# Optimization experiments

Measured on AMD Instinct MI355X. Metric: run time of the kernel, lower is better.

The kernel has to match this reference:

```python
import jax, jax.numpy as jnp
import numpy as np

S = 128            # image_size
NF = 64            # nf (channels)
B, N = 16, 1
DIM = S * S // 16  # 1024
HEADS = max(1, S // 16)  # 8
DH = DIM // HEADS  # 128


def setup_inputs() -> dict:
    key = jax.random.key(0)
    ks = jax.random.split(key, 10)
    sc = lambda fan_in: 1.0 / np.sqrt(fan_in)
    return {
        "x": jax.random.normal(ks[0], (B, N, NF, S, S), dtype=jnp.float32),
        "We": jax.random.uniform(ks[1], (DIM, S * S), jnp.float32, -sc(S * S), sc(S * S)),
        "be": jax.random.uniform(ks[2], (DIM,), jnp.float32, -sc(S * S), sc(S * S)),
        "pos": jax.random.normal(ks[3], (1, NF, DIM), dtype=jnp.float32),
        "Wq": jax.random.uniform(ks[4], (DIM, DIM), jnp.float32, -sc(DIM), sc(DIM)),
        "Wk": jax.random.uniform(ks[5], (NF, NF), jnp.float32, -sc(NF), sc(NF)),
        "Wv": jax.random.uniform(ks[6], (DIM, DIM), jnp.float32, -sc(DIM), sc(DIM)),
        "Wo": jax.random.uniform(ks[7], (S * S, DIM), jnp.float32, -sc(DIM), sc(DIM)),
        "bo": jax.random.uniform(ks[8], (S * S,), jnp.float32, -sc(DIM), sc(DIM)),
    }


def reference(x, We, be, pos, Wq, Wk, Wv, Wo, bo):
    b, n, C, H, W = x.shape
    bn = b * n
    xf = x.reshape(bn, C, H * W)                       # [BN, C, S^2]
    xe = jnp.einsum('bcp,dp->bcd', xf, We) + be + pos  # [BN, C, DIM]
    # q projection -> heads -> avgpool over head dim (AvgPool1d(dh) == mean)
    q = jnp.einsum('bcd,ed->bce', xe, Wq).reshape(bn, C, HEADS, DH)
    q = q.transpose(0, 2, 1, 3)                        # [BN, H, C, dh]
    q = q.mean(axis=-1)                                # [BN, H, C]
    k = jax.nn.sigmoid(jnp.einsum('bhc,fc->bhf', q, Wk))  # [BN, H, C]
    v = jnp.einsum('bcd,ed->bce', xe, Wv).reshape(bn, C, HEADS, DH)
    v = v.transpose(0, 2, 1, 3)                        # [BN, H, C, dh]
    # diag_embed(k) @ v == per-channel elementwise scale
    out = k[..., None] * v                             # [BN, H, C, dh]
    out = out.transpose(0, 2, 1, 3).reshape(bn, C, DIM)
    out = jnp.einsum('bcd,pd->bcp', out, Wo) + bo      # [BN, C, S^2]
    return out.reshape(b, n, C, H, W)
```

## Files before the change

kernel.cpp:

```cpp
#include <hip/hip_runtime.h>
#include <cstdint>
#include <cmath>


typedef __attribute__((ext_vector_type(8))) short short8;
typedef __attribute__((ext_vector_type(4))) float f32x4;

#define DIMD 1024
#define NCH  64
#define NHEAD 8
#define DHEAD 128

typedef __attribute__((address_space(1))) unsigned int gu32;
typedef __attribute__((address_space(3))) unsigned int lu32;

__device__ __forceinline__ void gload_lds16(const void* g, void* l) {
  __builtin_amdgcn_global_load_lds((gu32*)g, (lu32*)l, 16, 0, 0);
}

__device__ __forceinline__ unsigned short f2bf(float f) {
  union { float f; unsigned u; } a; a.f = f;
  unsigned u = a.u;
  unsigned r = (u + 0x7fffu + ((u >> 16) & 1u)) >> 16;
  return (unsigned short)r;
}
__device__ __forceinline__ float bf2f(unsigned short h) {
  union { unsigned u; float f; } a; a.u = ((unsigned)h) << 16; return a.f;
}

__global__ __launch_bounds__(256) void cvt_bf16_kernel(
    const float* __restrict__ in, unsigned short* __restrict__ out, int n8) {
  int i = blockIdx.x * 256 + threadIdx.x;
  if (i >= n8) return;
  const float4* p = (const float4*)in + (size_t)i * 2;
  float4 f0 = p[0], f1 = p[1];
  uint4 u;
  u.x = (unsigned)f2bf(f0.x) | ((unsigned)f2bf(f0.y) << 16);
  u.y = (unsigned)f2bf(f0.z) | ((unsigned)f2bf(f0.w) << 16);
  u.z = (unsigned)f2bf(f1.x) | ((unsigned)f2bf(f1.y) << 16);
  u.w = (unsigned)f2bf(f1.z) | ((unsigned)f2bf(f1.w) << 16);
  ((uint4*)out)[i] = u;
}

__global__ __launch_bounds__(256) void wqm2_kernel(
    const float* __restrict__ Wq, float* __restrict__ wqm) {
  int h = blockIdx.x >> 3, dbase = (blockIdx.x & 7) * 128;
  int d = threadIdx.x & 127, eh = threadIdx.x >> 7;
  const float* p = Wq + ((size_t)(h * DHEAD + eh * 64)) * DIMD + dbase + d;
  float s = 0.f;
  #pragma unroll 8
  for (int e = 0; e < 64; ++e) s += p[(size_t)e * DIMD];
  __shared__ float red[2][128];
  red[eh][d] = s;
  __syncthreads();
  if (eh == 0)
    wqm[h * DIMD + dbase + d] = (red[0][d] + red[1][d]) * (1.0f / DHEAD);
}

__global__ __launch_bounds__(256) void qk2_kernel(
    const unsigned short* __restrict__ xe, const float* __restrict__ wqm,
    const float* __restrict__ Wk, float* __restrict__ kout) {
  int b = blockIdx.x, h = blockIdx.y;
  int c = threadIdx.x & 63, dq = threadIdx.x >> 6;
  __shared__ float red[64][4];
  __shared__ float qs[64];
  const uint4* xr = (const uint4*)(xe + ((size_t)(b * NCH + c)) * DIMD + dq * 256);
  const float* wr = wqm + h * DIMD + dq * 256;
  float s = 0.f;
  #pragma unroll 4
  for (int i = 0; i < 32; ++i) {
    uint4 v = xr[i];
    s += bf2f((unsigned short)(v.x & 0xffff)) * wr[i * 8 + 0];
    s += bf2f((unsigned short)(v.x >> 16))    * wr[i * 8 + 1];
    s += bf2f((unsigned short)(v.y & 0xffff)) * wr[i * 8 + 2];
    s += bf2f((unsigned short)(v.y >> 16))    * wr[i * 8 + 3];
    s += bf2f((unsigned short)(v.z & 0xffff)) * wr[i * 8 + 4];
    s += bf2f((unsigned short)(v.z >> 16))    * wr[i * 8 + 5];
    s += bf2f((unsigned short)(v.w & 0xffff)) * wr[i * 8 + 6];
    s += bf2f((unsigned short)(v.w >> 16))    * wr[i * 8 + 7];
  }
  red[c][dq] = s;
  __syncthreads();
  if (dq == 0) qs[c] = red[c][0] + red[c][1] + red[c][2] + red[c][3];
  __syncthreads();
  int f = c;
  float s2 = 0.f;
  #pragma unroll
  for (int i = 0; i < 16; ++i) {
    int cc = dq * 16 + i;
    s2 += qs[cc] * Wk[f * NCH + cc];
  }
  red[f][dq] = s2;
  __syncthreads();
  if (dq == 0) {
    float q = red[f][0] + red[f][1] + red[f][2] + red[f][3];
    kout[(b * NHEAD + h) * NCH + f] = 1.f / (1.f + expf(-q));
  }
}

template<int MODE, int LAYOUT>
__global__ __launch_bounds__(256) void gemm_db(
    const unsigned short* __restrict__ A, const unsigned short* __restrict__ B,
    float* __restrict__ C, const float* __restrict__ bias,
    int M, int N, int K, int Ksub)
{
  __shared__ __align__(16) unsigned short As[2][128][32];
  __shared__ __align__(16) unsigned short Bs[2][128][32];

  const int bid = blockIdx.x;
  int m0, n0, kz;
  if (LAYOUT == 0) {
    kz = bid & 7; int r = bid >> 3; n0 = (r & 7) * 128; m0 = (r >> 3) * 128;
  } else if (LAYOUT == 1) {
    kz = (bid & 7) | (((bid >> 3) & 1) << 3);
    int r = bid >> 4; n0 = (r & 7) * 128; m0 = (r >> 3) * 128;
  } else {
    int nlo = bid & 7, nhi = bid >> 6;
    m0 = ((bid >> 3) & 7) * 128; n0 = (nlo + 8 * nhi) * 128; kz = 0;
  }

  const int tid  = threadIdx.x;
  const int lane = tid & 63, wave = tid >> 6;
  const int kbeg = kz * Ksub;
  const int lrow = lane >> 2;
  const int lcol = (lane & 3) * 8;
  const int q = lane >> 4, rl = lane & 15;
  const int wr = (wave >> 1) * 64, wc = (wave & 1) * 64;

  const unsigned short* ga = A + (size_t)(m0 + wave * 32 + lrow) * K + kbeg + lcol;
  const unsigned short* gb = B + (size_t)(n0 + wave * 32 + lrow) * K + kbeg + lcol;

  f32x4 acc[4][4] = {};

  gload_lds16(ga,                  &As[0][wave * 32][0]);
  gload_lds16(ga + (size_t)16 * K, &As[0][wave * 32 + 16][0]);
  gload_lds16(gb,                  &Bs[0][wave * 32][0]);
  gload_lds16(gb + (size_t)16 * K, &Bs[0][wave * 32 + 16][0]);
  ga += 32; gb += 32;

  int p = 0;
  for (int k0 = 0; k0 < Ksub; k0 += 32) {
    __syncthreads();
    if (k0 + 32 < Ksub) {
      gload_lds16(ga,                  &As[p ^ 1][wave * 32][0]);
      gload_lds16(ga + (size_t)16 * K, &As[p ^ 1][wave * 32 + 16][0]);
      gload_lds16(gb,                  &Bs[p ^ 1][wave * 32][0]);
      gload_lds16(gb + (size_t)16 * K, &Bs[p ^ 1][wave * 32 + 16][0]);
      ga += 32; gb += 32;
    }

    short8 af[4], bf[4];
    #pragma unroll
    for (int i = 0; i < 4; ++i)
      af[i] = *(const short8*)&As[p][wr + i * 16 + rl][q * 8];
    #pragma unroll
    for (int j = 0; j < 4; ++j)
      bf[j] = *(const short8*)&Bs[p][wc + j * 16 + rl][q * 8];
    #pragma unroll
    for (int i = 0; i < 4; ++i)
      #pragma unroll
      for (int j = 0; j < 4; ++j)
        acc[i][j] = __builtin_amdgcn_mfma_f32_16x16x32_bf16(af[i], bf[j], acc[i][j], 0, 0, 0);

    p ^= 1;
  }

  const size_t zoff = (MODE == 3) ? (size_t)kz * (size_t)M * (size_t)N : 0;
  #pragma unroll
  for (int i = 0; i < 4; ++i) {
    #pragma unroll
    for (int j = 0; j < 4; ++j) {
      #pragma unroll
      for (int r = 0; r < 4; ++r) {
        int row = m0 + wr + i * 16 + q * 4 + r;
        int col = n0 + wc + j * 16 + rl;
        if (MODE == 3) {
          C[zoff + (size_t)row * N + col] = acc[i][j][r];
        } else {
          C[(size_t)row * N + col] = acc[i][j][r] + bias[col];
        }
      }
    }
  }
}

template<int NS>
__global__ __launch_bounds__(256) void reduce1_kernel(
    const float* __restrict__ part, const float* __restrict__ be,
    const float* __restrict__ pos, unsigned short* __restrict__ xe) {
  int i = blockIdx.x * 256 + threadIdx.x;
  size_t base = (size_t)i * 4;
  int row = i >> 8, col = (i & 255) * 4;
  float4 s = {0.f, 0.f, 0.f, 0.f};
  #pragma unroll
  for (int sk = 0; sk < NS; ++sk) {
    float4 p = *(const float4*)(part + (size_t)sk * (DIMD * DIMD) + base);
    s.x += p.x; s.y += p.y; s.z += p.z; s.w += p.w;
  }
  float4 bv = *(const float4*)(be + col);
  float4 pv = *(const float4*)(pos + (size_t)(row & 63) * DIMD + col);
  uint2 u;
  u.x = (unsigned)f2bf(s.x + bv.x + pv.x) | ((unsigned)f2bf(s.y + bv.y + pv.y) << 16);
  u.y = (unsigned)f2bf(s.z + bv.z + pv.z) | ((unsigned)f2bf(s.w + bv.w + pv.w) << 16);
  *(uint2*)(xe + base) = u;
}

template<int NS>
__global__ __launch_bounds__(256) void reduce2_kernel(
    const float* __restrict__ part, const float* __restrict__ kv,
    unsigned short* __restrict__ t) {
  int i = blockIdx.x * 256 + threadIdx.x;
  size_t base = (size_t)i * 4;
  int row = i >> 8, col = (i & 255) * 4;
  float4 s = {0.f, 0.f, 0.f, 0.f};
  #pragma unroll
  for (int sk = 0; sk < NS; ++sk) {
    float4 p = *(const float4*)(part + (size_t)sk * (DIMD * DIMD) + base);
    s.x += p.x; s.y += p.y; s.z += p.z; s.w += p.w;
  }
  float sc = kv[((row >> 6) * NHEAD + (col >> 7)) * NCH + (row & 63)];
  uint2 u;
  u.x = (unsigned)f2bf(s.x * sc) | ((unsigned)f2bf(s.y * sc) << 16);
  u.y = (unsigned)f2bf(s.z * sc) | ((unsigned)f2bf(s.w * sc) << 16);
  *(uint2*)(t + base) = u;
}

template<int MODE, bool ABF16, int BM, int BN>
__global__ __launch_bounds__(256) void gemm_bt(
    const void* __restrict__ Ap, const float* __restrict__ B,
    void* __restrict__ C, const float* __restrict__ bias,
    const float* __restrict__ posp, const float* __restrict__ ksc,
    int M, int N, int K)
{
  constexpr int BK = 32;
  constexpr int LDR = BK + 8;
  __shared__ __align__(16) unsigned short As[BM][LDR];
  __shared__ __align__(16) unsigned short Bs[BN][LDR];

  const int tid = threadIdx.x;
  const int m0 = blockIdx.y * BM;
  const int n0 = blockIdx.x * BN;
  constexpr int EA = BM * BK / 256;
  constexpr int EB = BN * BK / 256;
  constexpr int MI = BM / 32;
  constexpr int NI = BN / 32;
  const int lane = tid & 63, wave = tid >> 6;
  const int wr = (wave >> 1) * (BM / 2);
  const int wc = (wave & 1) * (BN / 2);
  const int q = lane >> 4, rl = lane & 15;

  f32x4 acc[MI][NI] = {};

  for (int k0 = 0; k0 < K; k0 += BK) {
    {
      constexpr int CPR = BK / EA;
      int row = tid / CPR;
      int cs  = (tid % CPR) * EA;
      if (ABF16) {
        const unsigned short* a = (const unsigned short*)Ap + (size_t)(m0 + row) * K + k0 + cs;
        #pragma unroll
        for (int v = 0; v < EA / 8; ++v)
          *(uint4*)&As[row][cs + v * 8] = *(const uint4*)(a + v * 8);
      } else {
        const float* a = (const float*)Ap + (size_t)(m0 + row) * K + k0 + cs;
        #pragma unroll
        for (int v = 0; v < EA / 8; ++v) {
          float4 f0 = *(const float4*)(a + v * 8);
          float4 f1 = *(const float4*)(a + v * 8 + 4);
          uint4 u;
          u.x = (unsigned)f2bf(f0.x) | ((unsigned)f2bf(f0.y) << 16);
          u.y = (unsigned)f2bf(f0.z) | ((unsigned)f2bf(f0.w) << 16);
          u.z = (unsigned)f2bf(f1.x) | ((unsigned)f2bf(f1.y) << 16);
          u.w = (unsigned)f2bf(f1.z) | ((unsigned)f2bf(f1.w) << 16);
          *(uint4*)&As[row][cs + v * 8] = u;
        }
      }
    }
    {
      constexpr int CPR = BK / EB;
      int row = tid / CPR;
      int cs  = (tid % CPR) * EB;
      const float* b = B + (size_t)(n0 + row) * K + k0 + cs;
      #pragma unroll
      for (int v = 0; v < EB / 8; ++v) {
        float4 f0 = *(const float4*)(b + v * 8);
        float4 f1 = *(const float4*)(b + v * 8 + 4);
        uint4 u;
        u.x = (unsigned)f2bf(f0.x) | ((unsigned)f2bf(f0.y) << 16);
        u.y = (unsigned)f2bf(f0.z) | ((unsigned)f2bf(f0.w) << 16);
        u.z = (unsigned)f2bf(f1.x) | ((unsigned)f2bf(f1.y) << 16);
        u.w = (unsigned)f2bf(f1.z) | ((unsigned)f2bf(f1.w) << 16);
        *(uint4*)&Bs[row][cs + v * 8] = u;
      }
    }
    __syncthreads();

    short8 af[MI], bf[NI];
    #pragma unroll
    for (int i = 0; i < MI; ++i)
      af[i] = *(const short8*)&As[wr + i * 16 + rl][q * 8];
    #pragma unroll
    for (int j = 0; j < NI; ++j)
      bf[j] = *(const short8*)&Bs[wc + j * 16 + rl][q * 8];
    #pragma unroll
    for (int i = 0; i < MI; ++i)
      #pragma unroll
      for (int j = 0; j < NI; ++j)
        acc[i][j] = __builtin_amdgcn_mfma_f32_16x16x32_bf16(af[i], bf[j], acc[i][j], 0, 0, 0);

    __syncthreads();
  }

  #pragma unroll
  for (int i = 0; i < MI; ++i) {
    #pragma unroll
    for (int j = 0; j < NI; ++j) {
      #pragma unroll
      for (int r = 0; r < 4; ++r) {
        int row = m0 + wr + i * 16 + q * 4 + r;
        int col = n0 + wc + j * 16 + rl;
        float v = acc[i][j][r];
        if (MODE == 0) {
          v += bias[col] + posp[(size_t)(row & 63) * DIMD + col];
          ((unsigned short*)C)[(size_t)row * N + col] = f2bf(v);
        } else if (MODE == 1) {
          v *= ksc[((row >> 6) * NHEAD + (col >> 7)) * NCH + (row & 63)];
          ((unsigned short*)C)[(size_t)row * N + col] = f2bf(v);
        } else {
          ((float*)C)[(size_t)row * N + col] = v + bias[col];
        }
      }
    }
  }
}

__global__ void wqm_kernel(const float* __restrict__ Wq, float* __restrict__ wqm) {
  int h = blockIdx.x;
  for (int d = threadIdx.x; d < DIMD; d += 256) {
    float s = 0.f;
    const float* p = Wq + (size_t)h * DHEAD * DIMD + d;
    #pragma unroll 4
    for (int e = 0; e < DHEAD; ++e) s += p[(size_t)e * DIMD];
    wqm[h * DIMD + d] = s * (1.0f / DHEAD);
  }
}
__global__ void qk_kernel(const unsigned short* __restrict__ xe,
                          const float* __restrict__ wqm,
                          const float* __restrict__ Wk,
                          float* __restrict__ kout) {
  int b = blockIdx.x;
  __shared__ float qs[NHEAD][NCH];
  for (int t = threadIdx.x; t < NHEAD * NCH; t += 256) {
    int h = t >> 6, c = t & 63;
    const unsigned short* xr = xe + (size_t)(b * NCH + c) * DIMD;
    const float* wr = wqm + h * DIMD;
    float s = 0.f;
    #pragma unroll 8
    for (int d = 0; d < DIMD; ++d) s += bf2f(xr[d]) * wr[d];
    qs[h][c] = s;
  }
  __syncthreads();
  for (int t = threadIdx.x; t < NHEAD * NCH; t += 256) {
    int h = t >> 6, f = t & 63;
    float s = 0.f;
    #pragma unroll
    for (int c = 0; c < NCH; ++c) s += qs[h][c] * Wk[f * NCH + c];
    kout[b * (NHEAD * NCH) + h * NCH + f] = 1.f / (1.f + expf(-s));
  }
}

extern "C" void kernel_launch(void* const* d_in, const int* in_sizes, int n_in,
                              void* d_out, int out_size, void* d_ws, size_t ws_size,
                              hipStream_t stream) {
  const float* x   = (const float*)d_in[0];
  const float* We  = (const float*)d_in[1];
  const float* be  = (const float*)d_in[2];
  const float* pos = (const float*)d_in[3];
  const float* Wq  = (const float*)d_in[4];
  const float* Wk  = (const float*)d_in[5];
  const float* Wv  = (const float*)d_in[6];
  const float* Wo  = (const float*)d_in[7];
  const float* bo  = (const float*)d_in[8];
  float* out = (float*)d_out;

  const size_t MB = 1u << 20;
  const size_t WS16 = 102 * MB + 64 * 1024;
  const size_t WS8  = 70 * MB + 64 * 1024;

  if (ws_size >= WS16) {
    char* ws = (char*)d_ws;
    unsigned short* We_bf = (unsigned short*)(ws + 0);
    unsigned short* Wo_bf = (unsigned short*)(ws + 32 * MB);
    unsigned short* x_bf  = (unsigned short*)(ws + 64 * MB);
    unsigned short* Wv_bf = (unsigned short*)(ws + 96 * MB);
    unsigned short* xe    = (unsigned short*)(ws + 98 * MB);
    unsigned short* t     = (unsigned short*)(ws + 100 * MB);
    float* wqm = (float*)(ws + 102 * MB);
    float* kv  = (float*)(ws + 102 * MB + 32 * 1024);

    float* part1 = (float*)d_out;
    float* part2 = (float*)d_out;

    cvt_bf16_kernel<<<dim3(8192), 256, 0, stream>>>(x,  x_bf,  16777216 / 8);
    cvt_bf16_kernel<<<dim3(8192), 256, 0, stream>>>(We, We_bf, 16777216 / 8);
    cvt_bf16_kernel<<<dim3(512),  256, 0, stream>>>(Wv, Wv_bf, 1048576 / 8);
    cvt_bf16_kernel<<<dim3(8192), 256, 0, stream>>>(Wo, Wo_bf, 16777216 / 8);
    wqm2_kernel<<<dim3(64), 256, 0, stream>>>(Wq, wqm);

    gemm_db<3, 1><<<dim3(1024), 256, 0, stream>>>(
        x_bf, We_bf, part1, nullptr, 1024, 1024, 16384, 1024);
    reduce1_kernel<16><<<dim3(1024), 256, 0, stream>>>(part1, be, pos, xe);

    qk2_kernel<<<dim3(16, 8), 256, 0, stream>>>(xe, wqm, Wk, kv);

    gemm_db<3, 0><<<dim3(512), 256, 0, stream>>>(
        xe, Wv_bf, part2, nullptr, 1024, 1024, 1024, 128);
    reduce2_kernel<8><<<dim3(1024), 256, 0, stream>>>(part2, kv, t);

    gemm_db<2, 2><<<dim3(1024), 256, 0, stream>>>(
        t, Wo_bf, out, bo, 1024, 16384, 1024, 1024);
  } else if (ws_size >= WS8) {
    char* ws = (char*)d_ws;
    unsigned short* We_bf = (unsigned short*)(ws + 0);
    unsigned short* Wo_bf = (unsigned short*)(ws + 32 * MB);
    unsigned short* Wv_bf = (unsigned short*)(ws + 64 * MB);
    unsigned short* xe    = (unsigned short*)(ws + 66 * MB);
    unsigned short* t     = (unsigned short*)(ws + 68 * MB);
    float* wqm = (float*)(ws + 70 * MB);
    float* kv  = (float*)(ws + 70 * MB + 32 * 1024);

    char* ob = (char*)d_out;
    unsigned short* x_bf  = (unsigned short*)(ob + 0);
    float* part1 = (float*)(ob + 32 * MB);
    float* part2 = (float*)(ob + 0);

    cvt_bf16_kernel<<<dim3(8192), 256, 0, stream>>>(x,  x_bf,  16777216 / 8);
    cvt_bf16_kernel<<<dim3(8192), 256, 0, stream>>>(We, We_bf, 16777216 / 8);
    cvt_bf16_kernel<<<dim3(512),  256, 0, stream>>>(Wv, Wv_bf, 1048576 / 8);
    cvt_bf16_kernel<<<dim3(8192), 256, 0, stream>>>(Wo, Wo_bf, 16777216 / 8);
    wqm2_kernel<<<dim3(64), 256, 0, stream>>>(Wq, wqm);

    gemm_db<3, 0><<<dim3(512), 256, 0, stream>>>(
        x_bf, We_bf, part1, nullptr, 1024, 1024, 16384, 2048);
    reduce1_kernel<8><<<dim3(1024), 256, 0, stream>>>(part1, be, pos, xe);

    qk2_kernel<<<dim3(16, 8), 256, 0, stream>>>(xe, wqm, Wk, kv);

    gemm_db<3, 0><<<dim3(512), 256, 0, stream>>>(
        xe, Wv_bf, part2, nullptr, 1024, 1024, 1024, 128);
    reduce2_kernel<8><<<dim3(1024), 256, 0, stream>>>(part2, kv, t);

    gemm_db<2, 2><<<dim3(1024), 256, 0, stream>>>(
        t, Wo_bf, out, bo, 1024, 16384, 1024, 1024);
  } else {
    char* ws = (char*)d_ws;
    unsigned short* xe = (unsigned short*)ws;
    unsigned short* t  = (unsigned short*)(ws + (2u << 20));
    float* wqm = (float*)(ws + (4u << 20));
    float* kv  = (float*)(ws + (4u << 20) + (32u << 10));

    wqm_kernel<<<dim3(NHEAD), 256, 0, stream>>>(Wq, wqm);
    gemm_bt<0, false, 64, 64><<<dim3(16, 16), 256, 0, stream>>>(
        x, We, xe, be, pos, nullptr, 1024, 1024, 16384);
    qk_kernel<<<dim3(16), 256, 0, stream>>>(xe, wqm, Wk, kv);
    gemm_bt<1, true, 64, 64><<<dim3(16, 16), 256, 0, stream>>>(
        xe, Wv, t, nullptr, nullptr, kv, 1024, 1024, 1024);
    gemm_bt<2, true, 128, 128><<<dim3(128, 8), 256, 0, stream>>>(
        t, Wo, out, bo, nullptr, nullptr, 1024, 16384, 1024);
  }
}
```

Measured before the change: 368.6 us.

## Add 256x256 8-wave pipelined bf16 GEMM and fuse prep conversion kernels

Introduces a new GEMM kernel with 512 threads, 256x256 output tiles, K-step 64, swizzled LDS staging via global_load_lds, and a four-phase schedule that interleaves loads of the next tile with MFMA work on the current one. It is used for the two large GEMMs (x·We split-K and t·Wo) instead of the old 128x128 kernel. The five fp32-to-bf16 conversion and Wq-mean launches are merged into one kernel to cut launch overhead. The larger tiles reduce global traffic per FLOP but raise register and LDS pressure and leave fewer blocks to fill the CUs.

```diff
diff --git a/kernel.cpp b/kernel.cpp
--- a/kernel.cpp
+++ b/kernel.cpp
@@ -28,10 +28,8 @@
   union { unsigned u; float f; } a; a.u = ((unsigned)h) << 16; return a.f;
 }
 
-__global__ __launch_bounds__(256) void cvt_bf16_kernel(
-    const float* __restrict__ in, unsigned short* __restrict__ out, int n8) {
-  int i = blockIdx.x * 256 + threadIdx.x;
-  if (i >= n8) return;
+__device__ __forceinline__ void cvt8_body(const float* __restrict__ in,
+                                          unsigned short* __restrict__ out, int i) {
   const float4* p = (const float4*)in + (size_t)i * 2;
   float4 f0 = p[0], f1 = p[1];
   uint4 u;
@@ -40,6 +38,44 @@
   u.z = (unsigned)f2bf(f1.x) | ((unsigned)f2bf(f1.y) << 16);
   u.w = (unsigned)f2bf(f1.z) | ((unsigned)f2bf(f1.w) << 16);
   ((uint4*)out)[i] = u;
+}
+
+__global__ __launch_bounds__(256) void cvt_bf16_kernel(
+    const float* __restrict__ in, unsigned short* __restrict__ out, int n8) {
+  int i = blockIdx.x * 256 + threadIdx.x;
+  if (i >= n8) return;
+  cvt8_body(in, out, i);
+}
+
+__global__ __launch_bounds__(256) void prep_fused(
+    const float* __restrict__ x,  unsigned short* __restrict__ x_bf,
+    const float* __restrict__ We, unsigned short* __restrict__ We_bf,
+    const float* __restrict__ Wo, unsigned short* __restrict__ Wo_bf,
+    const float* __restrict__ Wv, unsigned short* __restrict__ Wv_bf,
+    const float* __restrict__ Wq, float* __restrict__ wqm) {
+  int b = blockIdx.x;
+  if (b < 8192) {
+    cvt8_body(x, x_bf, b * 256 + threadIdx.x);
+  } else if (b < 16384) {
+    cvt8_body(We, We_bf, (b - 8192) * 256 + threadIdx.x);
+  } else if (b < 24576) {
+    cvt8_body(Wo, Wo_bf, (b - 16384) * 256 + threadIdx.x);
+  } else if (b < 25088) {
+    cvt8_body(Wv, Wv_bf, (b - 24576) * 256 + threadIdx.x);
+  } else {
+    int bb = b - 25088;
+    int h = bb >> 3, dbase = (bb & 7) * 128;
+    int d = threadIdx.x & 127, eh = threadIdx.x >> 7;
+    const float* p = Wq + ((size_t)(h * DHEAD + eh * 64)) * DIMD + dbase + d;
+    float s = 0.f;
+    #pragma unroll 8
+    for (int e = 0; e < 64; ++e) s += p[(size_t)e * DIMD];
+    __shared__ float red[2][128];
+    red[eh][d] = s;
+    __syncthreads();
+    if (eh == 0)
+      wqm[h * DIMD + dbase + d] = (red[0][d] + red[1][d]) * (1.0f / DHEAD);
+  }
 }
 
 __global__ __launch_bounds__(256) void wqm2_kernel(
@@ -95,6 +131,121 @@
   if (dq == 0) {
     float q = red[f][0] + red[f][1] + red[f][2] + red[f][3];
     kout[(b * NHEAD + h) * NCH + f] = 1.f / (1.f + expf(-q));
+  }
+}
+
+
+#define BARR asm volatile("s_barrier" ::: "memory")
+#define VMW(n) asm volatile("s_waitcnt vmcnt(" #n ")" ::: "memory")
+#define ENDPH do { \
+  asm volatile("s_waitcnt lgkmcnt(0)" ::: "memory"); \
+  __builtin_amdgcn_sched_barrier(0); \
+  BARR; } while (0)
+
+#define SA(bb, kk, u) gload_lds16(gA + (size_t)(u) * 64 * K + (kk), \
+                                  lA0 + (bb) * 16384 + (u) * 4096)
+#define SB(bb, kk, u) gload_lds16(gB + (size_t)(u) * 64 * K + (kk), \
+                                  lB0 + (bb) * 16384 + (u) * 4096)
+
+#define PH(QM, QN, LOADA, STG) do { \
+  if (LOADA) { \
+    const unsigned short* ap = &As[buf][wm * 128 + (QM) * 64 + rl][0]; \
+    _Pragma("unroll") \
+    for (int i = 0; i < 4; ++i) { \
+      af0[i] = *(const short8*)(ap + i * 1024 + ((q ^ swz) << 3)); \
+      af1[i] = *(const short8*)(ap + i * 1024 + (((4 | q) ^ swz) << 3)); \
+    } \
+  } \
+  const unsigned short* bp = &Bs[buf][wn * 64 + (QN) * 32 + rl][0]; \
+  short8 b00 = *(const short8*)(bp + ((q ^ swz) << 3)); \
+  short8 b01 = *(const short8*)(bp + 1024 + ((q ^ swz) << 3)); \
+  short8 b10 = *(const short8*)(bp + (((4 | q) ^ swz) << 3)); \
+  short8 b11 = *(const short8*)(bp + 1024 + (((4 | q) ^ swz) << 3)); \
+  STG; \
+  BARR; \
+  __builtin_amdgcn_s_setprio(1); \
+  _Pragma("unroll") \
+  for (int i = 0; i < 4; ++i) { \
+    acc[(QM)*4+i][(QN)*2+0] = __builtin_amdgcn_mfma_f32_16x16x32_bf16(af0[i], b00, acc[(QM)*4+i][(QN)*2+0], 0, 0, 0); \
+    acc[(QM)*4+i][(QN)*2+0] = __builtin_amdgcn_mfma_f32_16x16x32_bf16(af1[i], b10, acc[(QM)*4+i][(QN)*2+0], 0, 0, 0); \
+    acc[(QM)*4+i][(QN)*2+1] = __builtin_amdgcn_mfma_f32_16x16x32_bf16(af0[i], b01, acc[(QM)*4+i][(QN)*2+1], 0, 0, 0); \
+    acc[(QM)*4+i][(QN)*2+1] = __builtin_amdgcn_mfma_f32_16x16x32_bf16(af1[i], b11, acc[(QM)*4+i][(QN)*2+1], 0, 0, 0); \
+  } \
+  __builtin_amdgcn_s_setprio(0); \
+  ENDPH; \
+} while (0)
+
+template<int MODE, int LAYOUT>
+__global__ __launch_bounds__(512, 2) void gemm8(
+    const unsigned short* __restrict__ A, const unsigned short* __restrict__ Bg,
+    float* __restrict__ C, const float* __restrict__ bias,
+    int M, int N, int K, int Ksub)
+{
+  __shared__ __align__(16) unsigned short As[2][256][64];
+  __shared__ __align__(16) unsigned short Bs[2][256][64];
+
+  const int bid = blockIdx.x;
+  int m0, n0, kz;
+  if (LAYOUT == 1) {
+    kz = (bid & 7) | (((bid >> 3) & 1) << 3);
+    int r = bid >> 4; n0 = (r & 3) * 256; m0 = (r >> 2) * 256;
+  } else {
+    int nlo = bid & 7; int r = bid >> 3;
+    m0 = (r & 3) * 256; n0 = (nlo + 8 * (r >> 2)) * 256; kz = 0;
+  }
+  const int kbeg = kz * Ksub;
+  const int NT = Ksub >> 6;
+
+  const int tid  = threadIdx.x;
+  const int lane = tid & 63, wave = tid >> 6;
+  const int wm = wave >> 2, wn = wave & 3;
+  const int q = lane >> 4, rl = lane & 15;
+  const int swz = rl & 7;
+
+  const int srow = wave * 8 + (lane >> 3);
+  const int kswz = ((lane & 7) ^ (lane >> 3)) << 3;
+  const unsigned short* gA = A  + (size_t)(m0 + srow) * K + kbeg + kswz;
+  const unsigned short* gB = Bg + (size_t)(n0 + srow) * K + kbeg + kswz;
+  unsigned short* lA0 = &As[0][0][0] + wave * 512;
+  unsigned short* lB0 = &Bs[0][0][0] + wave * 512;
+
+  f32x4 acc[8][4] = {};
+  short8 af0[4], af1[4];
+
+  SA(0, 0, 0); SA(0, 0, 2);
+  SB(0, 0, 0); SB(0, 0, 1); SB(0, 0, 2); SB(0, 0, 3);
+  SA(0, 0, 1); SA(0, 0, 3);
+  VMW(2);
+  BARR;
+
+  for (int t = 0; t < NT; ++t) {
+    const int buf = t & 1;
+    const int nb = buf ^ 1;
+    const bool s = (t + 1) < NT;
+    const size_t kn = (size_t)(t + 1) * 64;
+
+    PH(0, 0, true,  if (s) { SB(nb, kn, 0); SB(nb, kn, 1); });
+    PH(0, 1, false, if (s) { SB(nb, kn, 2); SB(nb, kn, 3); VMW(4); } else VMW(0));
+    PH(1, 0, true,  if (s) { SA(nb, kn, 0); SA(nb, kn, 2); });
+    PH(1, 1, false, if (s) { SA(nb, kn, 1); SA(nb, kn, 3); VMW(2); });
+  }
+
+  const size_t zoff = (MODE == 3) ? (size_t)kz * (size_t)M * (size_t)N : 0;
+  #pragma unroll
+  for (int mi = 0; mi < 8; ++mi) {
+    #pragma unroll
+    for (int nj = 0; nj < 4; ++nj) {
+      #pragma unroll
+      for (int r = 0; r < 4; ++r) {
+        int row = m0 + wm * 128 + mi * 16 + q * 4 + r;
+        int col = n0 + wn * 64 + nj * 16 + rl;
+        if (MODE == 3) {
+          C[zoff + (size_t)row * N + col] = acc[mi][nj][r];
+        } else {
+          C[(size_t)row * N + col] = acc[mi][nj][r] + bias[col];
+        }
+      }
+    }
   }
 }
 
@@ -401,13 +552,10 @@
     float* part1 = (float*)d_out;
     float* part2 = (float*)d_out;
 
-    cvt_bf16_kernel<<<dim3(8192), 256, 0, stream>>>(x,  x_bf,  16777216 / 8);
-    cvt_bf16_kernel<<<dim3(8192), 256, 0, stream>>>(We, We_bf, 16777216 / 8);
-    cvt_bf16_kernel<<<dim3(512),  256, 0, stream>>>(Wv, Wv_bf, 1048576 / 8);
-    cvt_bf16_kernel<<<dim3(8192), 256, 0, stream>>>(Wo, Wo_bf, 16777216 / 8);
-    wqm2_kernel<<<dim3(64), 256, 0, stream>>>(Wq, wqm);
-
-    gemm_db<3, 1><<<dim3(1024), 256, 0, stream>>>(
+    prep_fused<<<dim3(25152), 256, 0, stream>>>(
+        x, x_bf, We, We_bf, Wo, Wo_bf, Wv, Wv_bf, Wq, wqm);
+
+    gemm8<3, 1><<<dim3(256), 512, 0, stream>>>(
         x_bf, We_bf, part1, nullptr, 1024, 1024, 16384, 1024);
     reduce1_kernel<16><<<dim3(1024), 256, 0, stream>>>(part1, be, pos, xe);
 
@@ -417,7 +565,7 @@
         xe, Wv_bf, part2, nullptr, 1024, 1024, 1024, 128);
     reduce2_kernel<8><<<dim3(1024), 256, 0, stream>>>(part2, kv, t);
 
-    gemm_db<2, 2><<<dim3(1024), 256, 0, stream>>>(
+    gemm8<2, 2><<<dim3(256), 512, 0, stream>>>(
         t, Wo_bf, out, bo, 1024, 16384, 1024, 1024);
   } else if (ws_size >= WS8) {
     char* ws = (char*)d_ws;
```

After: 350.2 us. -5.0%, faster.
